# Kernel tuning notes

Measured on AMD Instinct MI355X. Metric: run time of the kernel, lower is better.

Reference implementation:

```python
import jax, jax.numpy as jnp
import numpy as np

B, C, H, W, NMAX = 16, 1, 128, 8192, 64


def setup_inputs() -> dict:
    key = jax.random.key(0)
    x = jax.random.normal(key, (B, C, H, W), dtype=jnp.float32)
    # Build realistic non-overlapping, sorted chirp boundaries with numpy.
    rng = np.random.default_rng(0)
    slot = W // NMAX  # 128 columns per chirp slot
    gaps = rng.integers(0, 40, size=(B, NMAX))
    widths = rng.integers(20, slot - 40, size=(B, NMAX))
    starts = np.arange(NMAX)[None, :] * slot + gaps
    ends = starts + widths
    n = rng.integers(48, NMAX + 1, size=(B,)).astype(np.int32)
    xi = np.stack([starts, ends], axis=-1).astype(np.int32)
    valid = np.arange(NMAX)[None, :] < n[:, None]
    xi = xi * valid[:, :, None]  # zero out invalid rows
    return {
        "x": x,
        "xi": jnp.asarray(xi),
        "N": jnp.asarray(n),
        "sep_param": jnp.zeros((1, 1, 1), dtype=jnp.float32),  # learned sep token scalar
    }


def reference(x, xi, N, sep_param):
    """Vectorized TinyBird.compactify_data: remove silence between chirp
    blocks, packing blocks contiguously with 1-column separators.
    Returns (x_new, xi_new). x_new keeps full width W (original truncates
    to data-dependent w_max; padding beyond w_max is zeros, same values)."""
    Bb, Cc, Hh, Ww = x.shape
    nmax = xi.shape[1]
    idx = jnp.arange(nmax, dtype=jnp.int32)[None, :]            # (1, Nmax)
    Nc = N.reshape(Bb, 1).astype(jnp.int32)                      # (B, 1)
    w = jnp.clip(xi[:, :, 1] - xi[:, :, 0], 0, None).astype(jnp.int32)
    valid = idx < Nc                                             # (B, Nmax)
    wv = jnp.where(valid, w, 0)
    csum = jnp.cumsum(wv, axis=1)
    start_new = csum - wv + idx                                  # compressed starts
    end_new = csum + idx                                         # compressed ends
    xi_new = jnp.where(valid[:, :, None],
                       jnp.stack([start_new, end_new], axis=-1), 0).astype(xi.dtype)

    # For every output column j, find which compressed segment it falls in.
    j = jnp.arange(Ww, dtype=jnp.int32)
    big = jnp.int32(Ww + nmax + 2)
    start_search = jnp.where(valid, start_new, big)              # keep sorted
    seg = jax.vmap(lambda s: jnp.searchsorted(s, j, side='right'))(start_search) - 1
    seg = jnp.clip(seg, 0, nmax - 1)                             # (B, W)
    bidx = jnp.arange(Bb)[:, None]
    s_new = start_new[bidx, seg]
    e_new = end_new[bidx, seg]
    seg_valid = valid[bidx, seg]
    in_seg = seg_valid & (j[None, :] >= s_new) & (j[None, :] < e_new)
    is_sep = seg_valid & (j[None, :] == e_new) & (seg < (Nc - 1))
    src = jnp.clip(xi[bidx, seg, 0].astype(jnp.int32) + (j[None, :] - s_new), 0, Ww - 1)
    src_full = jnp.broadcast_to(src[:, None, None, :], (Bb, Cc, Hh, Ww))
    gathered = jnp.take_along_axis(x, src_full, axis=3)          # ragged gather
    sep_val = sep_param[0, 0, 0]                                 # sep_token column value
    x_new = jnp.where(in_seg[:, None, None, :], gathered,
                      jnp.where(is_sep[:, None, None, :], sep_val, jnp.float32(0)))
    return x_new, xi_new
```

## Files before the change

kernel.cpp:

```cpp
#include <hip/hip_runtime.h>

#define Bn 16
#define Hn 128
#define Wn 8192
#define NMAX 64

typedef float nt_f4 __attribute__((ext_vector_type(4)));

__global__ void xi_new_kernel(const int* __restrict__ xi,
                              const int* __restrict__ N,
                              float* __restrict__ out_xi) {
    int b = blockIdx.x;
    int i = threadIdx.x;
    int nb = N[b];
    int s0 = xi[(b * NMAX + i) * 2 + 0];
    int s1 = xi[(b * NMAX + i) * 2 + 1];
    int w = s1 - s0; if (w < 0) w = 0;
    bool valid = i < nb;
    int wv = valid ? w : 0;
    int c = wv;
    #pragma unroll
    for (int d = 1; d < 64; d <<= 1) {
        int t = __shfl_up(c, d, 64);
        if (i >= d) c += t;
    }
    out_xi[(b * NMAX + i) * 2 + 0] = valid ? (float)(c - wv + i) : 0.0f;
    out_xi[(b * NMAX + i) * 2 + 1] = valid ? (float)(c + i) : 0.0f;
}

__global__ __launch_bounds__(256) void row_pack_kernel(
    const float* __restrict__ x, const int* __restrict__ xi,
    const int* __restrict__ N, const float* __restrict__ sep_param,
    float* __restrict__ out) {
    __shared__ int s_start[NMAX];
    __shared__ int s_w[NMAX];
    __shared__ int s_src0[NMAX];
    __shared__ int s_n, s_tail, s_wide;

    const int row = blockIdx.x;
    const int b   = row >> 7;
    const int tid = threadIdx.x;

    if (tid < NMAX) {
        int nb = N[b];
        int s0 = xi[(b * NMAX + tid) * 2 + 0];
        int s1 = xi[(b * NMAX + tid) * 2 + 1];
        int w = s1 - s0; if (w < 0) w = 0;
        bool valid = tid < nb;
        int wv = valid ? w : 0;
        int c = wv;
        #pragma unroll
        for (int d = 1; d < 64; d <<= 1) {
            int t = __shfl_up(c, d, 64);
            if (tid >= d) c += t;
        }
        int start_new = c - wv + tid;
        int end_new   = c + tid;
        s_start[tid] = start_new;
        s_w[tid]     = wv;
        s_src0[tid]  = s0;
        unsigned long long wide = __ballot(wv > 127);
        if (tid == 0) {
            s_n = nb;
            s_wide = (wide != 0ULL) ? 1 : 0;
        }
        int last = (nb > 0) ? (nb - 1) : 0;
        if (tid == last) s_tail = (nb > 0) ? end_new : 0;
    }
    __syncthreads();

    const int nb   = s_n;
    const int tail = s_tail;
    const float sep = sep_param[0];
    const float* __restrict__ xrow = x + (size_t)row * Wn;
    float* __restrict__ orow = out + (size_t)row * Wn;
    const int wave = tid >> 6;
    const int lane = tid & 63;

    float v0[16], v1[16];
    int sg_s[16], sg_wt[16];
    #pragma unroll
    for (int k = 0; k < 16; ++k) {
        const int seg = wave + 4 * k;
        const bool act = seg < nb;
        const int s    = act ? s_start[seg] : 0;
        const int w    = act ? s_w[seg] : 0;
        const int src0 = act ? s_src0[seg] : 0;
        sg_s[k]  = s;
        sg_wt[k] = act ? (w + ((seg < nb - 1) ? 1 : 0)) : 0;
        v0[k] = (lane < w)      ? xrow[src0 + lane]      : sep;
        v1[k] = (lane + 64 < w) ? xrow[src0 + lane + 64] : sep;
    }

    #pragma unroll
    for (int k = 0; k < 16; ++k) {
        if (lane < sg_wt[k])      orow[sg_s[k] + lane]      = v0[k];
        if (lane + 64 < sg_wt[k]) orow[sg_s[k] + lane + 64] = v1[k];
    }

    if (s_wide) {
        for (int seg = wave; seg < nb; seg += 4) {
            const int w = s_w[seg];
            const int wtot = w + ((seg < nb - 1) ? 1 : 0);
            for (int l = 128 + lane; l < wtot; l += 64) {
                orow[s_start[seg] + l] = (l < w) ? xrow[s_src0[seg] + l] : sep;
            }
        }
    }

    const int t4 = (tail + 3) & ~3;
    if (tid < (t4 - tail)) orow[tail + tid] = 0.0f;
    const nt_f4 z = {0.0f, 0.0f, 0.0f, 0.0f};
    nt_f4* orow4 = reinterpret_cast<nt_f4*>(orow);
    for (int i4 = (t4 >> 2) + tid; i4 < (Wn >> 2); i4 += 256) {
        __builtin_nontemporal_store(z, orow4 + i4);
    }
}

extern "C" void kernel_launch(void* const* d_in, const int* in_sizes, int n_in,
                              void* d_out, int out_size, void* d_ws, size_t ws_size,
                              hipStream_t stream) {
    const float* x   = (const float*)d_in[0];
    const int* xi    = (const int*)d_in[1];
    const int* N     = (const int*)d_in[2];
    const float* sep = (const float*)d_in[3];

    float* out_x  = (float*)d_out;
    float* out_xi = (float*)d_out + (size_t)Bn * Hn * Wn;

    xi_new_kernel<<<Bn, NMAX, 0, stream>>>(xi, N, out_xi);
    row_pack_kernel<<<Bn * Hn, 256, 0, stream>>>(x, xi, N, sep, out_x);
}
```

Before: 119.2 us.

## Stage packed row in LDS and write full row with coalesced vector stores

Each block now assembles its compacted output row in a 32 KB shared-memory buffer, scattering segment data and separators there, then writes the whole row to global memory with aligned float4 nontemporal stores. This replaces unaligned, partially masked scalar global stores with fully coalesced wide stores. The separate xi_new kernel is folded into the first block of each batch, saving one launch. The 32 KB of LDS per block may limit how many blocks fit on a CU and adds an extra barrier.

```diff
diff --git a/kernel.cpp b/kernel.cpp
--- a/kernel.cpp
+++ b/kernel.cpp
@@ -7,31 +7,11 @@
 
 typedef float nt_f4 __attribute__((ext_vector_type(4)));
 
-__global__ void xi_new_kernel(const int* __restrict__ xi,
-                              const int* __restrict__ N,
-                              float* __restrict__ out_xi) {
-    int b = blockIdx.x;
-    int i = threadIdx.x;
-    int nb = N[b];
-    int s0 = xi[(b * NMAX + i) * 2 + 0];
-    int s1 = xi[(b * NMAX + i) * 2 + 1];
-    int w = s1 - s0; if (w < 0) w = 0;
-    bool valid = i < nb;
-    int wv = valid ? w : 0;
-    int c = wv;
-    #pragma unroll
-    for (int d = 1; d < 64; d <<= 1) {
-        int t = __shfl_up(c, d, 64);
-        if (i >= d) c += t;
-    }
-    out_xi[(b * NMAX + i) * 2 + 0] = valid ? (float)(c - wv + i) : 0.0f;
-    out_xi[(b * NMAX + i) * 2 + 1] = valid ? (float)(c + i) : 0.0f;
-}
-
-__global__ __launch_bounds__(256) void row_pack_kernel(
+__global__ __launch_bounds__(256) void row_pack_lds_kernel(
     const float* __restrict__ x, const int* __restrict__ xi,
     const int* __restrict__ N, const float* __restrict__ sep_param,
-    float* __restrict__ out) {
+    float* __restrict__ out, float* __restrict__ out_xi) {
+    __shared__ float s_row[Wn];
     __shared__ int s_start[NMAX];
     __shared__ int s_w[NMAX];
     __shared__ int s_src0[NMAX];
@@ -66,6 +46,10 @@
         }
         int last = (nb > 0) ? (nb - 1) : 0;
         if (tid == last) s_tail = (nb > 0) ? end_new : 0;
+        if ((row & 127) == 0) {
+            out_xi[(b * NMAX + tid) * 2 + 0] = valid ? (float)start_new : 0.0f;
+            out_xi[(b * NMAX + tid) * 2 + 1] = valid ? (float)end_new : 0.0f;
+        }
     }
     __syncthreads();
 
@@ -94,8 +78,8 @@
 
     #pragma unroll
     for (int k = 0; k < 16; ++k) {
-        if (lane < sg_wt[k])      orow[sg_s[k] + lane]      = v0[k];
-        if (lane + 64 < sg_wt[k]) orow[sg_s[k] + lane + 64] = v1[k];
+        if (lane < sg_wt[k])      s_row[sg_s[k] + lane]      = v0[k];
+        if (lane + 64 < sg_wt[k]) s_row[sg_s[k] + lane + 64] = v1[k];
     }
 
     if (s_wide) {
@@ -103,17 +87,26 @@
             const int w = s_w[seg];
             const int wtot = w + ((seg < nb - 1) ? 1 : 0);
             for (int l = 128 + lane; l < wtot; l += 64) {
-                orow[s_start[seg] + l] = (l < w) ? xrow[s_src0[seg] + l] : sep;
+                s_row[s_start[seg] + l] = (l < w) ? xrow[s_src0[seg] + l] : sep;
             }
         }
     }
 
     const int t4 = (tail + 3) & ~3;
-    if (tid < (t4 - tail)) orow[tail + tid] = 0.0f;
-    const nt_f4 z = {0.0f, 0.0f, 0.0f, 0.0f};
+    if (tid < (t4 - tail)) s_row[tail + tid] = 0.0f;
+    float4* s_row4 = reinterpret_cast<float4*>(s_row);
+    const float4 z4 = make_float4(0.0f, 0.0f, 0.0f, 0.0f);
+    for (int i4 = (t4 >> 2) + tid; i4 < (Wn >> 2); i4 += 256) {
+        s_row4[i4] = z4;
+    }
+    __syncthreads();
+
     nt_f4* orow4 = reinterpret_cast<nt_f4*>(orow);
-    for (int i4 = (t4 >> 2) + tid; i4 < (Wn >> 2); i4 += 256) {
-        __builtin_nontemporal_store(z, orow4 + i4);
+    #pragma unroll
+    for (int g = 0; g < 8; ++g) {
+        float4 t = s_row4[g * 256 + tid];
+        nt_f4 v = {t.x, t.y, t.z, t.w};
+        __builtin_nontemporal_store(v, orow4 + g * 256 + tid);
     }
 }
 
@@ -128,6 +121,5 @@
     float* out_x  = (float*)d_out;
     float* out_xi = (float*)d_out + (size_t)Bn * Hn * Wn;
 
-    xi_new_kernel<<<Bn, NMAX, 0, stream>>>(xi, N, out_xi);
-    row_pack_kernel<<<Bn * Hn, 256, 0, stream>>>(x, xi, N, sep, out_x);
+    row_pack_lds_kernel<<<Bn * Hn, 256, 0, stream>>>(x, xi, N, sep, out_x, out_xi);
 }
```

Result: faster. 114.9 us, median of 2 (-3.6%).
